# Performance work log

Hardware: AMD Instinct MI355X
Metric: run time of the kernel (lower is better)

Reference implementation:

```python
import jax, jax.numpy as jnp
import numpy as np

N_NODES = 50000
N_EDGES = 800000
IN_DIM = 128
HID = 128
OUT_DIM = 40
N_EXP = 4


def setup_inputs() -> dict:
    key = jax.random.key(0)
    ks = jax.random.split(key, 20)
    def lin(k, o, i, scale=None):
        s = scale if scale is not None else 1.0 / np.sqrt(i)
        return jax.random.uniform(k, (o, i), jnp.float32, -s, s)
    inp = {}
    inp['x'] = jax.random.normal(ks[0], (N_NODES, IN_DIM), jnp.float32)
    inp['edge_index'] = jax.random.randint(ks[1], (2, N_EDGES), 0, N_NODES, jnp.int64)
    # layer 0: in=IN_DIM -> HID ; layer 1: in=HID -> HID
    dims = [(IN_DIM, HID), (HID, HID)]
    for l, (ci, co) in enumerate(dims):
        inp[f'lin_w{l}'] = lin(ks[2 + 6 * l], co, ci)
        inp[f'lin_b{l}'] = jnp.zeros((co,), jnp.float32)
        inp[f'agg_w{l}'] = jax.random.uniform(ks[3 + 6 * l], (N_EXP, co, ci + co), jnp.float32, -1.0 / np.sqrt(ci + co), 1.0 / np.sqrt(ci + co))
        inp[f'agg_b{l}'] = jnp.zeros((N_EXP, co), jnp.float32)
        inp[f'gate_w{l}'] = lin(ks[4 + 6 * l], N_EXP, ci + co)
        inp[f'gate_b{l}'] = jnp.zeros((N_EXP,), jnp.float32)
    inp['post_w1'] = lin(ks[16], HID, HID)
    inp['post_b1'] = jnp.zeros((HID,), jnp.float32)
    inp['post_w2'] = lin(ks[17], OUT_DIM, HID)
    inp['post_b2'] = jnp.zeros((OUT_DIM,), jnp.float32)
    return inp


def _sage_layer(x, src, dst, lin_w, lin_b, agg_w, agg_b, gate_w, gate_b):
    n = x.shape[0]
    # message: gather source nodes, linear + relu  [E, out]
    msg = jax.nn.relu(x[src] @ lin_w.T + lin_b)
    # mean aggregation over destination nodes (empty -> 0, as in PyG)
    s = jax.ops.segment_sum(msg, dst, num_segments=n)
    cnt = jax.ops.segment_sum(jnp.ones((src.shape[0], 1), msg.dtype), dst, num_segments=n)
    aggr = s / jnp.maximum(cnt, 1.0)
    # update: gated mixture of 4 expert linears over concat(x, aggr)
    xc = jnp.concatenate([x, aggr], axis=1)            # [N, in+out]
    gate = jax.nn.softmax(xc @ gate_w.T + gate_b, axis=1)  # [N, E]
    exp = jax.nn.relu(jnp.einsum('nc,eoc->neo', xc, agg_w) + agg_b)  # [N, E, out]
    out = jnp.einsum('neo,ne->no', exp, gate)
    # F.normalize(p=2, dim=1, eps=1e-12)
    nrm = jnp.linalg.norm(out, axis=1, keepdims=True)
    return out / jnp.maximum(nrm, 1e-12)


def reference(x, edge_index,
              lin_w0, lin_b0, agg_w0, agg_b0, gate_w0, gate_b0,
              lin_w1, lin_b1, agg_w1, agg_b1, gate_w1, gate_b1,
              post_w1, post_b1, post_w2, post_b2):
    src, dst = edge_index[0], edge_index[1]
    h = _sage_layer(x, src, dst, lin_w0, lin_b0, agg_w0, agg_b0, gate_w0, gate_b0)
    h = jax.nn.relu(h)  # dropout p=0.0 -> identity
    h = _sage_layer(h, src, dst, lin_w1, lin_b1, agg_w1, agg_b1, gate_w1, gate_b1)
    h = jax.nn.relu(h)
    h = h @ post_w1.T + post_b1
    h = h @ post_w2.T + post_b2
    return jax.nn.log_softmax(h, axis=1)
```

## Files before the change

### kernel.cpp

```cpp
#include <hip/hip_runtime.h>
#include <hip/hip_bf16.h>
#include <cmath>

#define NN 50000
#define NE 800000
#define NBLK_SCAN 196

typedef __attribute__((ext_vector_type(4))) float f32x4;
typedef __attribute__((ext_vector_type(8))) short bfx8;

__device__ inline ushort f2bf(float x) {
  return __bfloat16_as_ushort(__float2bfloat16(x));
}

#define BAR_NODRAIN() asm volatile("s_waitcnt lgkmcnt(0)\ns_barrier" ::: "memory")

__global__ void count_kernel(const int* __restrict__ dst, unsigned int* __restrict__ cnt) {
  int e = blockIdx.x * 256 + threadIdx.x;
  if (e < NE) atomicAdd(&cnt[dst[e]], 1u);
}

__global__ void partial_kernel(const unsigned int* __restrict__ cnt,
                               unsigned int* __restrict__ bsum) {
  __shared__ unsigned int s[256];
  const int t = threadIdx.x;
  const int i = blockIdx.x * 256 + t;
  s[t] = (i < NN) ? cnt[i] : 0u;
  __syncthreads();
#pragma unroll
  for (int o = 128; o > 0; o >>= 1) {
    if (t < o) s[t] += s[t + o];
    __syncthreads();
  }
  if (t == 0) bsum[blockIdx.x] = s[0];
}

__global__ void scanb_kernel(unsigned int* __restrict__ bsum) {
  __shared__ unsigned int s[256];
  const int t = threadIdx.x;
  const unsigned int v = (t < NBLK_SCAN) ? bsum[t] : 0u;
  s[t] = v;
  __syncthreads();
  for (int o = 1; o < 256; o <<= 1) {
    unsigned int u = (t >= o) ? s[t - o] : 0u;
    __syncthreads();
    s[t] += u;
    __syncthreads();
  }
  if (t < NBLK_SCAN) bsum[t] = s[t] - v;
}

__global__ void apply_kernel(unsigned int* __restrict__ cnt,
                             const unsigned int* __restrict__ bsum,
                             unsigned int* __restrict__ rowstart) {
  __shared__ unsigned int s[256];
  const int t = threadIdx.x;
  const int i = blockIdx.x * 256 + t;
  const unsigned int v = (i < NN) ? cnt[i] : 0u;
  s[t] = v;
  __syncthreads();
  for (int o = 1; o < 256; o <<= 1) {
    unsigned int u = (t >= o) ? s[t - o] : 0u;
    __syncthreads();
    s[t] += u;
    __syncthreads();
  }
  const unsigned int excl = s[t] - v + bsum[blockIdx.x];
  if (i < NN) {
    rowstart[i] = excl;
    cnt[i] = excl;
    if (i == NN - 1) rowstart[NN] = excl + v;
  }
}

__global__ void bucket_kernel(const int* __restrict__ src, const int* __restrict__ dst,
                              unsigned int* __restrict__ cursor, int* __restrict__ esrc) {
  int e = blockIdx.x * 256 + threadIdx.x;
  if (e < NE) {
    unsigned int pos = atomicAdd(&cursor[dst[e]], 1u);
    esrc[pos] = src[e];
  }
}

__global__ void wconv_kernel(const float* __restrict__ w, ushort* __restrict__ hi,
                             ushort* __restrict__ lo, int count) {
  int i = blockIdx.x * 256 + threadIdx.x;
  if (i < count) {
    float x = w[i];
    ushort h = f2bf(x);
    float hf = __uint_as_float(((unsigned int)h) << 16);
    hi[i] = h;
    lo[i] = f2bf(x - hf);
  }
}

__global__ __launch_bounds__(256) void aggregate_kernel(const float* __restrict__ A,
                                                        const int* __restrict__ esrc,
                                                        const unsigned int* __restrict__ rowstart,
                                                        float* __restrict__ S) {
  const int t = blockIdx.x * 256 + threadIdx.x;
  const int node = t >> 5;
  const int lane = t & 31;
  if (node >= NN) return;
  const unsigned int rs = rowstart[node], re = rowstart[node + 1];
  f32x4 acc = (f32x4){0.f, 0.f, 0.f, 0.f};
  unsigned int j = rs;
  for (; j + 4 <= re; j += 4) {
    const int s0 = esrc[j], s1 = esrc[j + 1], s2 = esrc[j + 2], s3 = esrc[j + 3];
    const f32x4 v0 = *(const f32x4*)&A[(size_t)s0 * 128 + lane * 4];
    const f32x4 v1 = *(const f32x4*)&A[(size_t)s1 * 128 + lane * 4];
    const f32x4 v2 = *(const f32x4*)&A[(size_t)s2 * 128 + lane * 4];
    const f32x4 v3 = *(const f32x4*)&A[(size_t)s3 * 128 + lane * 4];
    acc += (v0 + v1) + (v2 + v3);
  }
  for (; j < re; ++j) {
    const int s = esrc[j];
    acc += *(const f32x4*)&A[(size_t)s * 128 + lane * 4];
  }
  const float inv = 1.0f / fmaxf((float)(re - rs), 1.0f);
  *(f32x4*)&S[(size_t)node * 128 + lane * 4] = acc * inv;
}

template <int RELU>
__global__ __launch_bounds__(256, 3) void linm_kernel(const float* __restrict__ in,
                                                      const ushort* __restrict__ Whi,
                                                      const ushort* __restrict__ Wlo,
                                                      const float* __restrict__ bias,
                                                      float* __restrict__ out) {
  __shared__ __align__(16) ushort Ahi[64 * 64];
  __shared__ __align__(16) ushort Alo[64 * 64];
  __shared__ __align__(16) ushort Bhi[128 * 64];
  __shared__ __align__(16) ushort Blo[128 * 64];
  __shared__ float bs[128];

  const int tid = threadIdx.x;
  const int nb = blockIdx.x * 64;
  const int lane = tid & 63;
  const int wv = tid >> 6;
  const int cl = lane & 15;
  const int kg = lane >> 4;

  if (tid < 128) bs[tid] = bias[tid];

  f32x4 aP[4];
  bfx8 bP[2][8];

#pragma unroll
  for (int q = 0; q < 2; ++q) {
    const int task = tid + q * 256, row = task >> 3, g = task & 7;
    const int n = min(nb + row, NN - 1);
    aP[q * 2 + 0] = __builtin_nontemporal_load((const f32x4*)&in[(size_t)n * 128 + g * 8]);
    aP[q * 2 + 1] = __builtin_nontemporal_load((const f32x4*)&in[(size_t)n * 128 + g * 8 + 4]);
  }
#pragma unroll
  for (int q = 0; q < 4; ++q) {
    const int task = tid + q * 256, o = task >> 3, g = task & 7;
    bP[0][q * 2 + 0] = *(const bfx8*)&Whi[o * 128 + g * 8];
    bP[0][q * 2 + 1] = *(const bfx8*)&Wlo[o * 128 + g * 8];
  }

  f32x4 acc[4][2];
#pragma unroll
  for (int m = 0; m < 4; ++m)
#pragma unroll
    for (int f = 0; f < 2; ++f) acc[m][f] = (f32x4){0.f, 0.f, 0.f, 0.f};

#pragma unroll
  for (int c = 0; c < 2; ++c) {
    BAR_NODRAIN();
    {
#pragma unroll
      for (int q = 0; q < 2; ++q) {
        const int task = tid + q * 256, row = task >> 3, g = task & 7;
        const f32x4 v0 = aP[q * 2 + 0], v1 = aP[q * 2 + 1];
        const float vv[8] = {v0[0], v0[1], v0[2], v0[3], v1[0], v1[1], v1[2], v1[3]};
        bfx8 hv, lv;
#pragma unroll
        for (int i = 0; i < 8; ++i) {
          ushort h = f2bf(vv[i]);
          float hf = __uint_as_float(((unsigned int)h) << 16);
          hv[i] = (short)h;
          lv[i] = (short)f2bf(vv[i] - hf);
        }
        const int gsw = (g ^ (row & 7)) * 8;
        *(bfx8*)&Ahi[row * 64 + gsw] = hv;
        *(bfx8*)&Alo[row * 64 + gsw] = lv;
      }
    }
    {
#pragma unroll
      for (int q = 0; q < 4; ++q) {
        const int task = tid + q * 256, o = task >> 3, g = task & 7;
        const int gsw = (g ^ (o & 7)) * 8;
        *(bfx8*)&Bhi[o * 64 + gsw] = bP[c][q * 2 + 0];
        *(bfx8*)&Blo[o * 64 + gsw] = bP[c][q * 2 + 1];
      }
    }
    if (c == 0) {
#pragma unroll
      for (int q = 0; q < 2; ++q) {
        const int task = tid + q * 256, row = task >> 3, g = task & 7;
        const int n = min(nb + row, NN - 1);
        aP[q * 2 + 0] = __builtin_nontemporal_load((const f32x4*)&in[(size_t)n * 128 + 64 + g * 8]);
        aP[q * 2 + 1] = __builtin_nontemporal_load((const f32x4*)&in[(size_t)n * 128 + 64 + g * 8 + 4]);
      }
#pragma unroll
      for (int q = 0; q < 4; ++q) {
        const int task = tid + q * 256, o = task >> 3, g = task & 7;
        bP[1][q * 2 + 0] = *(const bfx8*)&Whi[o * 128 + 64 + g * 8];
        bP[1][q * 2 + 1] = *(const bfx8*)&Wlo[o * 128 + 64 + g * 8];
      }
    }
    BAR_NODRAIN();
#pragma unroll
    for (int ks = 0; ks < 2; ++ks) {
      bfx8 ah[4], al[4];
#pragma unroll
      for (int m = 0; m < 4; ++m) {
        const int ar = m * 16 + cl;
        const int gi = ((ks * 4 + kg) ^ (ar & 7)) * 8;
        ah[m] = *(const bfx8*)&Ahi[ar * 64 + gi];
        al[m] = *(const bfx8*)&Alo[ar * 64 + gi];
      }
#pragma unroll
      for (int f = 0; f < 2; ++f) {
        const int o = wv * 32 + f * 16 + cl;
        const int gi = ((ks * 4 + kg) ^ (o & 7)) * 8;
        const bfx8 bh = *(const bfx8*)&Bhi[o * 64 + gi];
        const bfx8 bl = *(const bfx8*)&Blo[o * 64 + gi];
#pragma unroll
        for (int m = 0; m < 4; ++m) {
          acc[m][f] = __builtin_amdgcn_mfma_f32_16x16x32_bf16(ah[m], bh, acc[m][f], 0, 0, 0);
          acc[m][f] = __builtin_amdgcn_mfma_f32_16x16x32_bf16(ah[m], bl, acc[m][f], 0, 0, 0);
          acc[m][f] = __builtin_amdgcn_mfma_f32_16x16x32_bf16(al[m], bh, acc[m][f], 0, 0, 0);
        }
      }
    }
  }

#pragma unroll
  for (int m = 0; m < 4; ++m) {
#pragma unroll
    for (int r = 0; r < 4; ++r) {
      const int node = m * 16 + kg * 4 + r;
      const int n = nb + node;
      if (n >= NN) continue;
#pragma unroll
      for (int f = 0; f < 2; ++f) {
        const int col = wv * 32 + f * 16 + cl;
        float v = acc[m][f][r] + bs[col];
        if (RELU) v = fmaxf(v, 0.f);
        out[(size_t)n * 128 + col] = v;
      }
    }
  }
}

__global__ __launch_bounds__(512, 2) void update_kernel(
    const float* __restrict__ xin, const float* __restrict__ S,
    const float* __restrict__ gw, const float* __restrict__ gb,
    const ushort* __restrict__ Whi, const ushort* __restrict__ Wlo,
    const float* __restrict__ aggb, float* __restrict__ hout) {
  __shared__ __align__(16) ushort Ahi[64 * 256];
  __shared__ __align__(16) ushort Alo[64 * 256];
  __shared__ __align__(16) ushort Bhi[128 * 64];
  __shared__ __align__(16) ushort Blo[128 * 64];
  __shared__ float wgs[1024];
  __shared__ float gbs[4];
  __shared__ float aggbs[512];
  __shared__ float gts[256];
  __shared__ float red[4 * 64];

  const int tid = threadIdx.x;
  const int nb = blockIdx.x * 64;
  const int lane = tid & 63;
  const int wv = tid >> 6;
  const int wr = wv >> 2;
  const int wc = wv & 3;
  const int cl = lane & 15;
  const int kg = lane >> 4;

  for (int i = tid; i < 1024; i += 512) wgs[i] = gw[i];
  if (tid < 512) aggbs[tid] = aggb[tid];
  if (tid < 4) gbs[tid] = gb[tid];

  const int r0 = tid >> 5;
  const int ga = tid & 31;
  f32x4 aL[4][2];
#pragma unroll
  for (int q = 0; q < 4; ++q) {
    const int row = r0 + q * 16;
    const int n = min(nb + row, NN - 1);
    const float* sp = (ga < 16) ? (xin + (size_t)n * 128 + ga * 8)
                                : (S + (size_t)n * 128 + (ga - 16) * 8);
    aL[q][0] = __builtin_nontemporal_load((const f32x4*)sp);
    aL[q][1] = __builtin_nontemporal_load((const f32x4*)(sp + 4));
  }
  bfx8 bPh[2], bPl[2];
#pragma unroll
  for (int q = 0; q < 2; ++q) {
    const int task = tid + q * 512;
    const int o = task >> 3, g = task & 7;
    bPh[q] = *(const bfx8*)&Whi[o * 256 + g * 8];
    bPl[q] = *(const bfx8*)&Wlo[o * 256 + g * 8];
  }
  __syncthreads();

  float gacc[4][4];
#pragma unroll
  for (int q = 0; q < 4; ++q)
#pragma unroll
    for (int e = 0; e < 4; ++e) gacc[q][e] = 0.f;
#pragma unroll
  for (int q = 0; q < 4; ++q) {
    const int row = r0 + q * 16;
    const f32x4 v0 = aL[q][0], v1 = aL[q][1];
    const float vv[8] = {v0[0], v0[1], v0[2], v0[3], v1[0], v1[1], v1[2], v1[3]};
    bfx8 hv, lv;
#pragma unroll
    for (int i = 0; i < 8; ++i) {
      const int k = ga * 8 + i;
#pragma unroll
      for (int e = 0; e < 4; ++e) gacc[q][e] += vv[i] * wgs[e * 256 + k];
      ushort h = f2bf(vv[i]);
      float hf = __uint_as_float(((unsigned int)h) << 16);
      hv[i] = (short)h;
      lv[i] = (short)f2bf(vv[i] - hf);
    }
    const int gsw = (ga ^ (row & 7)) * 8;
    *(bfx8*)&Ahi[row * 256 + gsw] = hv;
    *(bfx8*)&Alo[row * 256 + gsw] = lv;
  }
#pragma unroll
  for (int q = 0; q < 4; ++q) {
#pragma unroll
    for (int mask = 1; mask < 32; mask <<= 1) {
#pragma unroll
      for (int e = 0; e < 4; ++e) gacc[q][e] += __shfl_xor(gacc[q][e], mask);
    }
  }
  if ((tid & 31) == 0) {
#pragma unroll
    for (int q = 0; q < 4; ++q) {
      const int row = r0 + q * 16;
      float g0 = gacc[q][0] + gbs[0], g1 = gacc[q][1] + gbs[1];
      float g2 = gacc[q][2] + gbs[2], g3 = gacc[q][3] + gbs[3];
      float m = fmaxf(fmaxf(g0, g1), fmaxf(g2, g3));
      float e0 = expf(g0 - m), e1 = expf(g1 - m), e2 = expf(g2 - m), e3 = expf(g3 - m);
      float si = 1.0f / (e0 + e1 + e2 + e3);
      gts[row * 4 + 0] = e0 * si;
      gts[row * 4 + 1] = e1 * si;
      gts[row * 4 + 2] = e2 * si;
      gts[row * 4 + 3] = e3 * si;
    }
  }

  f32x4 res[2][2];
#pragma unroll
  for (int m = 0; m < 2; ++m)
#pragma unroll
    for (int f = 0; f < 2; ++f) res[m][f] = (f32x4){0.f, 0.f, 0.f, 0.f};

#pragma unroll
  for (int e = 0; e < 4; ++e) {
    f32x4 acc[2][2];
#pragma unroll
    for (int m = 0; m < 2; ++m)
#pragma unroll
      for (int f = 0; f < 2; ++f) acc[m][f] = (f32x4){0.f, 0.f, 0.f, 0.f};

#pragma unroll
    for (int c = 0; c < 4; ++c) {
      BAR_NODRAIN();
      {
#pragma unroll
        for (int q = 0; q < 2; ++q) {
          const int task = tid + q * 512;
          const int o = task >> 3, g = task & 7;
          const int gsw = (g ^ (o & 7)) * 8;
          *(bfx8*)&Bhi[o * 64 + gsw] = bPh[q];
          *(bfx8*)&Blo[o * 64 + gsw] = bPl[q];
        }
      }
      {
        const int pn = e * 4 + c + 1;
        if (pn < 16) {
          const int pe = pn >> 2, pc = pn & 3;
#pragma unroll
          for (int q = 0; q < 2; ++q) {
            const int task = tid + q * 512;
            const int o = task >> 3, g = task & 7;
            bPh[q] = *(const bfx8*)&Whi[pe * 32768 + o * 256 + pc * 64 + g * 8];
            bPl[q] = *(const bfx8*)&Wlo[pe * 32768 + o * 256 + pc * 64 + g * 8];
          }
        }
      }
      BAR_NODRAIN();
#pragma unroll
      for (int ks = 0; ks < 2; ++ks) {
        bfx8 ah[2], al[2];
#pragma unroll
        for (int m = 0; m < 2; ++m) {
          const int ar = wr * 32 + m * 16 + cl;
          const int gi = ((c * 8 + ks * 4 + kg) ^ (ar & 7)) * 8;
          ah[m] = *(const bfx8*)&Ahi[ar * 256 + gi];
          al[m] = *(const bfx8*)&Alo[ar * 256 + gi];
        }
#pragma unroll
        for (int f = 0; f < 2; ++f) {
          const int o = wc * 32 + f * 16 + cl;
          const int gi = ((ks * 4 + kg) ^ (o & 7)) * 8;
          const bfx8 bh = *(const bfx8*)&Bhi[o * 64 + gi];
          const bfx8 bl = *(const bfx8*)&Blo[o * 64 + gi];
#pragma unroll
          for (int m = 0; m < 2; ++m) {
            acc[m][f] = __builtin_amdgcn_mfma_f32_16x16x32_bf16(ah[m], bh, acc[m][f], 0, 0, 0);
            acc[m][f] = __builtin_amdgcn_mfma_f32_16x16x32_bf16(ah[m], bl, acc[m][f], 0, 0, 0);
            acc[m][f] = __builtin_amdgcn_mfma_f32_16x16x32_bf16(al[m], bh, acc[m][f], 0, 0, 0);
          }
        }
      }
    }
    const float b0 = aggbs[e * 128 + wc * 32 + cl];
    const float b1 = aggbs[e * 128 + wc * 32 + 16 + cl];
#pragma unroll
    for (int m = 0; m < 2; ++m) {
#pragma unroll
      for (int r = 0; r < 4; ++r) {
        const int node = wr * 32 + m * 16 + kg * 4 + r;
        const float g = gts[node * 4 + e];
        res[m][0][r] += g * fmaxf(acc[m][0][r] + b0, 0.f);
        res[m][1][r] += g * fmaxf(acc[m][1][r] + b1, 0.f);
      }
    }
  }

#pragma unroll
  for (int m = 0; m < 2; ++m) {
    f32x4 ss;
#pragma unroll
    for (int r = 0; r < 4; ++r)
      ss[r] = res[m][0][r] * res[m][0][r] + res[m][1][r] * res[m][1][r];
#pragma unroll
    for (int mask = 1; mask < 16; mask <<= 1) {
#pragma unroll
      for (int r = 0; r < 4; ++r) ss[r] += __shfl_xor(ss[r], mask);
    }
    if (cl == 0) {
#pragma unroll
      for (int r = 0; r < 4; ++r) red[wc * 64 + wr * 32 + m * 16 + kg * 4 + r] = ss[r];
    }
  }
  __syncthreads();
#pragma unroll
  for (int m = 0; m < 2; ++m) {
#pragma unroll
    for (int r = 0; r < 4; ++r) {
      const int node = wr * 32 + m * 16 + kg * 4 + r;
      const int n = nb + node;
      if (n >= NN) continue;
      const float t = red[node] + red[64 + node] + red[128 + node] + red[192 + node];
      const float inv = 1.0f / fmaxf(sqrtf(t), 1e-12f);
      hout[(size_t)n * 128 + wc * 32 + cl]      = fmaxf(res[m][0][r] * inv, 0.f);
      hout[(size_t)n * 128 + wc * 32 + 16 + cl] = fmaxf(res[m][1][r] * inv, 0.f);
    }
  }
}

__global__ void post2_kernel(const float* __restrict__ P, const float* __restrict__ W2,
                             const float* __restrict__ b2, float* __restrict__ out) {
  __shared__ __align__(16) float ps[32 * 132];
  __shared__ __align__(16) float w2s[40 * 132];
  __shared__ float b2s[40];
  const int tid = threadIdx.x;
  const int nb = blockIdx.x * 32;
  for (int i = tid; i < 5120; i += 256) {
    int o = i >> 7, k = i & 127;
    w2s[o * 132 + k] = W2[i];
  }
  if (tid < 40) b2s[tid] = b2[tid];
  {
    const int k = tid & 127;
    const int nl0 = tid >> 7;
#pragma unroll
    for (int r = 0; r < 16; ++r) {
      int nl = r * 2 + nl0;
      int n = min(nb + nl, NN - 1);
      ps[nl * 132 + k] = P[n * 128 + k];
    }
  }
  __syncthreads();

  const int nl = tid >> 3, g = tid & 7;
  float acc[5] = {0.f, 0.f, 0.f, 0.f, 0.f};
  for (int k = 0; k < 128; k += 4) {
    const float4 pv = *(const float4*)&ps[nl * 132 + k];
#pragma unroll
    for (int j = 0; j < 5; ++j) {
      const int o = g * 5 + j;
      const float4 wv = *(const float4*)&w2s[o * 132 + k];
      acc[j] += pv.x * wv.x + pv.y * wv.y + pv.z * wv.z + pv.w * wv.w;
    }
  }
  float l[5];
  float m = -1e30f;
#pragma unroll
  for (int j = 0; j < 5; ++j) {
    l[j] = acc[j] + b2s[g * 5 + j];
    m = fmaxf(m, l[j]);
  }
  m = fmaxf(m, __shfl_xor(m, 1, 8));
  m = fmaxf(m, __shfl_xor(m, 2, 8));
  m = fmaxf(m, __shfl_xor(m, 4, 8));
  float s = 0.f;
#pragma unroll
  for (int j = 0; j < 5; ++j) s += expf(l[j] - m);
  s += __shfl_xor(s, 1, 8);
  s += __shfl_xor(s, 2, 8);
  s += __shfl_xor(s, 4, 8);
  const float lse = m + logf(s);
  const int n = nb + nl;
  if (n < NN) {
#pragma unroll
    for (int j = 0; j < 5; ++j) out[n * 40 + g * 5 + j] = l[j] - lse;
  }
}

extern "C" void kernel_launch(void* const* d_in, const int* in_sizes, int n_in,
                              void* d_out, int out_size, void* d_ws, size_t ws_size,
                              hipStream_t stream) {
  const float* x       = (const float*)d_in[0];
  const int*   ei      = (const int*)d_in[1];
  const int*   src     = ei;
  const int*   dstp    = ei + NE;
  const float* lin_w0  = (const float*)d_in[2];
  const float* lin_b0  = (const float*)d_in[3];
  const float* agg_w0  = (const float*)d_in[4];
  const float* agg_b0  = (const float*)d_in[5];
  const float* gate_w0 = (const float*)d_in[6];
  const float* gate_b0 = (const float*)d_in[7];
  const float* lin_w1  = (const float*)d_in[8];
  const float* lin_b1  = (const float*)d_in[9];
  const float* agg_w1  = (const float*)d_in[10];
  const float* agg_b1  = (const float*)d_in[11];
  const float* gate_w1 = (const float*)d_in[12];
  const float* gate_b1 = (const float*)d_in[13];
  const float* post_w1 = (const float*)d_in[14];
  const float* post_b1 = (const float*)d_in[15];
  const float* post_w2 = (const float*)d_in[16];
  const float* post_b2 = (const float*)d_in[17];

  float* A  = (float*)d_ws;
  float* Sb = A + 6400000;
  float* H1 = Sb + 6400000;
  ushort* WHIa = (ushort*)(H1 + 6400000);
  ushort* WLOa = WHIa + 262144;
  ushort* WHIl = WLOa + 262144;
  ushort* WLOl = WHIl + 49152;
  unsigned int* CNT      = (unsigned int*)(WLOl + 49152);
  unsigned int* ROWSTART = CNT + NN;
  unsigned int* BSUM     = ROWSTART + NN + 1;
  int*          ESRC     = (int*)(BSUM + 256);

  const int gridN64 = (NN + 63) / 64;

  (void)hipMemsetAsync(CNT, 0, NN * sizeof(unsigned int), stream);
  count_kernel<<<NE / 256, 256, 0, stream>>>(dstp, CNT);
  partial_kernel<<<NBLK_SCAN, 256, 0, stream>>>(CNT, BSUM);
  scanb_kernel<<<1, 256, 0, stream>>>(BSUM);
  apply_kernel<<<NBLK_SCAN, 256, 0, stream>>>(CNT, BSUM, ROWSTART);
  bucket_kernel<<<NE / 256, 256, 0, stream>>>(src, dstp, CNT, ESRC);
  wconv_kernel<<<512, 256, 0, stream>>>(agg_w0, WHIa, WLOa, 131072);
  wconv_kernel<<<512, 256, 0, stream>>>(agg_w1, WHIa + 131072, WLOa + 131072, 131072);
  wconv_kernel<<<64, 256, 0, stream>>>(lin_w0, WHIl, WLOl, 16384);
  wconv_kernel<<<64, 256, 0, stream>>>(lin_w1, WHIl + 16384, WLOl + 16384, 16384);
  wconv_kernel<<<64, 256, 0, stream>>>(post_w1, WHIl + 32768, WLOl + 32768, 16384);

  linm_kernel<1><<<gridN64, 256, 0, stream>>>(x, WHIl, WLOl, lin_b0, A);
  aggregate_kernel<<<(NN * 32 + 255) / 256, 256, 0, stream>>>(A, ESRC, ROWSTART, Sb);
  update_kernel<<<gridN64, 512, 0, stream>>>(x, Sb, gate_w0, gate_b0, WHIa, WLOa, agg_b0, H1);

  linm_kernel<1><<<gridN64, 256, 0, stream>>>(H1, WHIl + 16384, WLOl + 16384, lin_b1, A);
  aggregate_kernel<<<(NN * 32 + 255) / 256, 256, 0, stream>>>(A, ESRC, ROWSTART, Sb);
  update_kernel<<<gridN64, 512, 0, stream>>>(H1, Sb, gate_w1, gate_b1, WHIa + 131072,
                                             WLOa + 131072, agg_b1, A);

  linm_kernel<0><<<gridN64, 256, 0, stream>>>(A, WHIl + 32768, WLOl + 32768, post_b1, Sb);
  post2_kernel<<<(NN + 31) / 32, 256, 0, stream>>>(Sb, post_w2, post_b2, (float*)d_out);
}
```

Before: 591.1 us.

## Read expert weights directly from global memory instead of staging through LDS

Removes the Bhi/Blo shared-memory tiles and their register prefetch in update_kernel, so each wave loads its B fragments straight from global (L2-resident) expert weights. This drops two barriers per K-chunk and frees LDS, and launch bounds are raised to allow 4 blocks per CU. The cost is more global/L2 load traffic per wave, since weight fragments are now fetched redundantly by each wave row. There is also less latency hiding, because the B loads are no longer prefetched a step ahead.

```diff
diff --git a/kernel.cpp b/kernel.cpp
--- a/kernel.cpp
+++ b/kernel.cpp
@@ -256,15 +256,13 @@
   }
 }
 
-__global__ __launch_bounds__(512, 2) void update_kernel(
+__global__ __launch_bounds__(512, 4) void update_kernel(
     const float* __restrict__ xin, const float* __restrict__ S,
     const float* __restrict__ gw, const float* __restrict__ gb,
     const ushort* __restrict__ Whi, const ushort* __restrict__ Wlo,
     const float* __restrict__ aggb, float* __restrict__ hout) {
   __shared__ __align__(16) ushort Ahi[64 * 256];
   __shared__ __align__(16) ushort Alo[64 * 256];
-  __shared__ __align__(16) ushort Bhi[128 * 64];
-  __shared__ __align__(16) ushort Blo[128 * 64];
   __shared__ float wgs[1024];
   __shared__ float gbs[4];
   __shared__ float aggbs[512];
@@ -295,14 +293,6 @@
                                 : (S + (size_t)n * 128 + (ga - 16) * 8);
     aL[q][0] = __builtin_nontemporal_load((const f32x4*)sp);
     aL[q][1] = __builtin_nontemporal_load((const f32x4*)(sp + 4));
-  }
-  bfx8 bPh[2], bPl[2];
-#pragma unroll
-  for (int q = 0; q < 2; ++q) {
-    const int task = tid + q * 512;
-    const int o = task >> 3, g = task & 7;
-    bPh[q] = *(const bfx8*)&Whi[o * 256 + g * 8];
-    bPl[q] = *(const bfx8*)&Wlo[o * 256 + g * 8];
   }
   __syncthreads();
 
@@ -354,6 +344,7 @@
       gts[row * 4 + 3] = e3 * si;
     }
   }
+  __syncthreads();
 
   f32x4 res[2][2];
 #pragma unroll
@@ -363,6 +354,8 @@
 
 #pragma unroll
   for (int e = 0; e < 4; ++e) {
+    const ushort* wh = Whi + e * 32768;
+    const ushort* wl = Wlo + e * 32768;
     f32x4 acc[2][2];
 #pragma unroll
     for (int m = 0; m < 2; ++m)
@@ -371,31 +364,6 @@
 
 #pragma unroll
     for (int c = 0; c < 4; ++c) {
-      BAR_NODRAIN();
-      {
-#pragma unroll
-        for (int q = 0; q < 2; ++q) {
-          const int task = tid + q * 512;
-          const int o = task >> 3, g = task & 7;
-          const int gsw = (g ^ (o & 7)) * 8;
-          *(bfx8*)&Bhi[o * 64 + gsw] = bPh[q];
-          *(bfx8*)&Blo[o * 64 + gsw] = bPl[q];
-        }
-      }
-      {
-        const int pn = e * 4 + c + 1;
-        if (pn < 16) {
-          const int pe = pn >> 2, pc = pn & 3;
-#pragma unroll
-          for (int q = 0; q < 2; ++q) {
-            const int task = tid + q * 512;
-            const int o = task >> 3, g = task & 7;
-            bPh[q] = *(const bfx8*)&Whi[pe * 32768 + o * 256 + pc * 64 + g * 8];
-            bPl[q] = *(const bfx8*)&Wlo[pe * 32768 + o * 256 + pc * 64 + g * 8];
-          }
-        }
-      }
-      BAR_NODRAIN();
 #pragma unroll
       for (int ks = 0; ks < 2; ++ks) {
         bfx8 ah[2], al[2];
@@ -406,12 +374,12 @@
           ah[m] = *(const bfx8*)&Ahi[ar * 256 + gi];
           al[m] = *(const bfx8*)&Alo[ar * 256 + gi];
         }
+        const int kgo = c * 64 + (ks * 4 + kg) * 8;
 #pragma unroll
         for (int f = 0; f < 2; ++f) {
           const int o = wc * 32 + f * 16 + cl;
-          const int gi = ((ks * 4 + kg) ^ (o & 7)) * 8;
-          const bfx8 bh = *(const bfx8*)&Bhi[o * 64 + gi];
-          const bfx8 bl = *(const bfx8*)&Blo[o * 64 + gi];
+          const bfx8 bh = *(const bfx8*)&wh[o * 256 + kgo];
+          const bfx8 bl = *(const bfx8*)&wl[o * 256 + kgo];
 #pragma unroll
           for (int m = 0; m < 2; ++m) {
             acc[m][f] = __builtin_amdgcn_mfma_f32_16x16x32_bf16(ah[m], bh, acc[m][f], 0, 0, 0);
```

New measurement: 693.0 us. +17.3%, slower.
